# Kernel optimization log

Measured on AMD Instinct MI355X. Metric: run time of the kernel, lower is better.

## Reference

```python
import jax, jax.numpy as jnp
import numpy as np

B, V, S = 16, 100000, 4096
LOSS_WEIGHT = 1.0


def setup_inputs() -> dict:
    key = jax.random.key(0)
    k1, k2, k3, k4 = jax.random.split(key, 4)
    return {
        "src_verts": jax.random.normal(k1, (B, V, 3), dtype=jnp.float32),
        "dst_verts": jax.random.normal(k2, (B, V, 3), dtype=jnp.float32),
        "src_idx": jax.random.randint(k3, (B, S), 0, V, dtype=jnp.int64),
        "dst_idx": jax.random.randint(k4, (B, S), 0, V, dtype=jnp.int64),
    }


def _gather(verts, idx):
    # verts: (B, V, 3), idx: (B, S) -> (B, S, 3)
    return jnp.take_along_axis(verts, idx[:, :, None], axis=1)


def reference(src_verts, dst_verts, src_idx, dst_idx):
    src = _gather(src_verts, src_idx)  # (B, S, 3)
    dst = _gather(dst_verts, dst_idx)  # (B, S, 3)
    # squared euclidean distance matrix, matching torch.cdist(p=2)**2
    s2 = jnp.sum(src * src, axis=-1)  # (B, S)
    d2 = jnp.sum(dst * dst, axis=-1)  # (B, S)
    gram = jnp.einsum("bsc,btc->bst", src, dst)  # (B, S, S)
    dist_mat = jnp.maximum(s2[:, :, None] + d2[:, None, :] - 2.0 * gram, 0.0)
    # min over src points (dim=1) + min over dst points (dim=2)
    chamfer_distance = jnp.min(dist_mat, axis=1) + jnp.min(dist_mat, axis=2)  # (B, S)
    chamfer_loss = jnp.mean(chamfer_distance, axis=-1)  # (B,)
    chamfer_loss = jnp.mean(chamfer_loss, axis=0)  # scalar ('mean' reduction)
    return chamfer_loss * LOSS_WEIGHT
```

## Files before the change

### kernel.cpp

```cpp
#include <hip/hip_runtime.h>
#include <hip/hip_bf16.h>
#include <math.h>

#define B 16
#define V 100000
#define S 4096
#define BS (B * S)
#define NT 512
#define JP 16
#define ONE_BF 0x3F80u

typedef __attribute__((ext_vector_type(8))) short bf16x8;
typedef __attribute__((ext_vector_type(16))) float f32x16;

static __device__ __forceinline__ unsigned bft(float x) {
  return __float_as_uint(x) >> 16;
}
static __device__ __forceinline__ float bff(unsigned hbits) {
  return __uint_as_float(hbits << 16);
}
static __device__ __forceinline__ unsigned pk(unsigned lo, unsigned hi) {
  return (lo & 0xFFFFu) | (hi << 16);
}


__global__ __launch_bounds__(NT) void chamfer_prep_kernel(
    const float* __restrict__ src_verts, const float* __restrict__ dst_verts,
    const int* __restrict__ src_idx, const int* __restrict__ dst_idx,
    uint2* __restrict__ srcfrag, uint4* __restrict__ dstfrag,
    float* __restrict__ out) {
  int t = blockIdx.x * NT + threadIdx.x;
  if (t == 0) *out = 0.f;
  int set = t >> 16;
  int i = t & (BS - 1);
  int b = i >> 12;

  const int* idx = set ? dst_idx : src_idx;
  const float* verts = set ? dst_verts : src_verts;
  int v = idx[i];
  v = v < 0 ? 0 : (v >= V ? V - 1 : v);
  const float* pv = verts + ((size_t)b * V + v) * 3;
  float x = pv[0], y = pv[1], z = pv[2];
  unsigned hx = bft(x), hy = bft(y), hz = bft(z);
  float n2 = x * x + y * y + z * z;
  unsigned n2h = bft(n2);
  unsigned n2l = bft(n2 - bff(n2h));

  if (set == 0) {
    unsigned lx = bft(x - bff(hx)), ly = bft(y - bff(hy)), lz = bft(z - bff(hz));
    int tile = i >> 5, c = i & 31;
    uint2* base = srcfrag + (size_t)tile * 128;
    base[c]      = make_uint2(pk(hx, hy), pk(hz, lx));
    base[64 + c] = make_uint2(pk(ly, lz), pk(hx, hy));
    base[32 + c] = make_uint2(pk(hz, n2h), pk(n2l, ONE_BF));
    base[96 + c] = make_uint2(pk(ONE_BF, 0u), 0u);
  } else {
    unsigned mx = bft(-2.f * bff(hx)), my = bft(-2.f * bff(hy)), mz = bft(-2.f * bff(hz));
    unsigned nx = bft(-2.f * (x - bff(hx)));
    unsigned ny = bft(-2.f * (y - bff(hy)));
    unsigned nz = bft(-2.f * (z - bff(hz)));
    dstfrag[(size_t)i * 2]     = make_uint4(pk(mx, my), pk(mz, mx), pk(my, mz), pk(nx, ny));
    dstfrag[(size_t)i * 2 + 1] = make_uint4(pk(nz, ONE_BF), pk(ONE_BF, n2h), pk(n2l, 0u), 0u);
  }
}

__global__ __launch_bounds__(NT, 4) void chamfer_mfma_kernel(
    const uint4* __restrict__ srcfrag4, const uint4* __restrict__ dstfrag,
    float* __restrict__ part_src, float* __restrict__ part_dst) {
  __shared__ struct {
    uint4 sfrag[2048];
    unsigned smin[1024];
  } sh;
  float* red = (float*)sh.sfrag;

  int bid = blockIdx.x;
  int b = bid >> 6;
  int jp = (bid >> 2) & 15;
  int iq = bid & 3;
  int tid = threadIdx.x;

  const uint4* chunk = srcfrag4 + (size_t)(b * S + iq * 1024) * 2;
  #pragma unroll
  for (int k = 0; k < 4; ++k) {
    sh.sfrag[tid + k * NT] = chunk[tid + k * NT];
  }
  for (int p = tid; p < 1024; p += NT) sh.smin[p] = 0x7F800000u;

  int w = tid >> 6;
  int lane = tid & 63;
  int c = lane & 31, h = lane >> 5;
  int gj = b * S + jp * 256 + w * 32 + c;
  bf16x8 A = __builtin_bit_cast(bf16x8, dstfrag[(size_t)gj * 2 + h]);

  __syncthreads();

  const uint2* sf2 = (const uint2*)sh.sfrag;
  f32x16 zero = {};
  f32x16 mn;
  #pragma unroll
  for (int r = 0; r < 16; ++r) mn[r] = INFINITY;

  int t0r = 4 * w;
  #pragma unroll 4
  for (int it = 0; it < 32; ++it) {
    int t = (it + t0r) & 31;
    uint2 u0 = sf2[t * 128 + lane];
    uint2 u1 = sf2[t * 128 + 64 + lane];
    bf16x8 Bf = __builtin_bit_cast(bf16x8, make_uint4(u0.x, u0.y, u1.x, u1.y));
    f32x16 d = __builtin_amdgcn_mfma_f32_32x32x16_bf16(A, Bf, zero, 0, 0, 0);
    #pragma unroll
    for (int r = 0; r < 16; ++r) mn[r] = fminf(mn[r], d[r]);
    float t0 = fminf(fminf(d[0], d[1]), d[2]);
    float t1 = fminf(fminf(d[3], d[4]), d[5]);
    float t2 = fminf(fminf(d[6], d[7]), d[8]);
    float t3 = fminf(fminf(d[9], d[10]), d[11]);
    float t4 = fminf(fminf(d[12], d[13]), d[14]);
    float m = fminf(fminf(fminf(t0, t1), fminf(t2, t3)), fminf(t4, d[15]));
    atomicMin(&sh.smin[t * 32 + c], __float_as_uint(fmaxf(m, 0.f)));
  }

  __syncthreads();
  for (int p = tid; p < 1024; p += NT) {
    part_src[jp * BS + b * S + iq * 1024 + p] = __uint_as_float(sh.smin[p]);
  }
  __syncthreads();

  #pragma unroll
  for (int r = 0; r < 16; ++r) {
    int row = w * 32 + (r & 3) + 8 * (r >> 2) + 4 * h;
    red[row * 33 + c] = mn[r];
  }
  __syncthreads();
  {
    int row = tid >> 1, half = tid & 1;
    const float* rp = red + row * 33 + half * 16;
    float a0 = fminf(fminf(rp[0], rp[1]), rp[2]);
    float a1 = fminf(fminf(rp[3], rp[4]), rp[5]);
    float a2 = fminf(fminf(rp[6], rp[7]), rp[8]);
    float a3 = fminf(fminf(rp[9], rp[10]), rp[11]);
    float a4 = fminf(fminf(rp[12], rp[13]), rp[14]);
    float m = fminf(fminf(fminf(a0, a1), fminf(a2, a3)), fminf(a4, rp[15]));
    m = fminf(m, __shfl_xor(m, 1, 64));
    if (half == 0) {
      part_dst[iq * BS + b * S + jp * 256 + row] = fmaxf(m, 0.f);
    }
  }
}

__global__ __launch_bounds__(256) void chamfer_reduce_kernel(
    const float* __restrict__ parts, float* __restrict__ out) {
  __shared__ float red[4];
  int tid = threadIdx.x;
  int i4 = blockIdx.x * 256 + tid;

  const float4* ps = (const float4*)parts;
  const float4* pd = (const float4*)(parts + 16 * BS);

  float4 ms = ps[i4];
  #pragma unroll
  for (int j = 1; j < 16; ++j) {
    float4 t = ps[j * (BS / 4) + i4];
    ms.x = fminf(ms.x, t.x); ms.y = fminf(ms.y, t.y);
    ms.z = fminf(ms.z, t.z); ms.w = fminf(ms.w, t.w);
  }
  float4 md = pd[i4];
  #pragma unroll
  for (int j = 1; j < 4; ++j) {
    float4 t = pd[j * (BS / 4) + i4];
    md.x = fminf(md.x, t.x); md.y = fminf(md.y, t.y);
    md.z = fminf(md.z, t.z); md.w = fminf(md.w, t.w);
  }
  float v = (ms.x + ms.y + ms.z + ms.w) + (md.x + md.y + md.z + md.w);
  v *= (1.0f / (float)BS);

  #pragma unroll
  for (int off = 32; off > 0; off >>= 1) v += __shfl_down(v, off, 64);
  if ((tid & 63) == 0) red[tid >> 6] = v;
  __syncthreads();
  if (tid == 0) atomicAdd(out, (red[0] + red[1]) + (red[2] + red[3]));
}

extern "C" void kernel_launch(void* const* d_in, const int* in_sizes, int n_in,
                              void* d_out, int out_size, void* d_ws, size_t ws_size,
                              hipStream_t stream) {
  const float* src_verts = (const float*)d_in[0];
  const float* dst_verts = (const float*)d_in[1];
  const int* src_idx = (const int*)d_in[2];
  const int* dst_idx = (const int*)d_in[3];
  float* out = (float*)d_out;

  float* parts = (float*)d_ws;
  float* part_src = parts;
  float* part_dst = parts + 16 * BS;
  uint2* srcfrag = (uint2*)(parts + 21 * BS);
  uint4* dstfrag = (uint4*)(parts + 29 * BS);

  chamfer_prep_kernel<<<2 * BS / NT, NT, 0, stream>>>(
      src_verts, dst_verts, src_idx, dst_idx, srcfrag, dstfrag, out);

  chamfer_mfma_kernel<<<B * JP * 4, NT, 0, stream>>>(
      (const uint4*)srcfrag, dstfrag, part_src, part_dst);

  chamfer_reduce_kernel<<<64, 256, 0, stream>>>(parts, out);
}
```

Baseline: 33.19 us.

## Compute two MFMA row tiles per wave with 256 threads and one 16-byte B fragment read

The MFMA kernel now runs 256 threads per block. Each wave holds two A fragments covering 64 dst rows, so every B fragment read from LDS feeds two MFMAs. The src fragment layout is repacked so each lane loads a single uint4 instead of two uint2 values, and one atomicMin per tile now covers both MFMAs. The aim is to cut LDS traffic and LDS atomics per unit of MFMA work, at the cost of more accumulator registers and fewer waves per block.

```diff
diff --git a/kernel.cpp b/kernel.cpp
--- a/kernel.cpp
+++ b/kernel.cpp
@@ -6,8 +6,7 @@
 #define V 100000
 #define S 4096
 #define BS (B * S)
-#define NT 512
-#define JP 16
+#define NT 256
 #define ONE_BF 0x3F80u
 
 typedef __attribute__((ext_vector_type(8))) short bf16x8;
@@ -24,12 +23,12 @@
 }
 
 
-__global__ __launch_bounds__(NT) void chamfer_prep_kernel(
+__global__ __launch_bounds__(512) void chamfer_prep_kernel(
     const float* __restrict__ src_verts, const float* __restrict__ dst_verts,
     const int* __restrict__ src_idx, const int* __restrict__ dst_idx,
-    uint2* __restrict__ srcfrag, uint4* __restrict__ dstfrag,
+    uint4* __restrict__ srcfrag, uint4* __restrict__ dstfrag,
     float* __restrict__ out) {
-  int t = blockIdx.x * NT + threadIdx.x;
+  int t = blockIdx.x * 512 + threadIdx.x;
   if (t == 0) *out = 0.f;
   int set = t >> 16;
   int i = t & (BS - 1);
@@ -49,11 +48,9 @@
   if (set == 0) {
     unsigned lx = bft(x - bff(hx)), ly = bft(y - bff(hy)), lz = bft(z - bff(hz));
     int tile = i >> 5, c = i & 31;
-    uint2* base = srcfrag + (size_t)tile * 128;
-    base[c]      = make_uint2(pk(hx, hy), pk(hz, lx));
-    base[64 + c] = make_uint2(pk(ly, lz), pk(hx, hy));
-    base[32 + c] = make_uint2(pk(hz, n2h), pk(n2l, ONE_BF));
-    base[96 + c] = make_uint2(pk(ONE_BF, 0u), 0u);
+    uint4* base = srcfrag + (size_t)tile * 64;
+    base[c]      = make_uint4(pk(hx, hy), pk(hz, lx), pk(ly, lz), pk(hx, hy));
+    base[32 + c] = make_uint4(pk(hz, n2h), pk(n2l, ONE_BF), pk(ONE_BF, 0u), 0u);
   } else {
     unsigned mx = bft(-2.f * bff(hx)), my = bft(-2.f * bff(hy)), mz = bft(-2.f * bff(hz));
     unsigned nx = bft(-2.f * (x - bff(hx)));
@@ -65,7 +62,7 @@
 }
 
 __global__ __launch_bounds__(NT, 4) void chamfer_mfma_kernel(
-    const uint4* __restrict__ srcfrag4, const uint4* __restrict__ dstfrag,
+    const uint4* __restrict__ srcfrag, const uint4* __restrict__ dstfrag,
     float* __restrict__ part_src, float* __restrict__ part_dst) {
   __shared__ struct {
     uint4 sfrag[2048];
@@ -79,71 +76,88 @@
   int iq = bid & 3;
   int tid = threadIdx.x;
 
-  const uint4* chunk = srcfrag4 + (size_t)(b * S + iq * 1024) * 2;
-  #pragma unroll
-  for (int k = 0; k < 4; ++k) {
+  const uint4* chunk = srcfrag + (size_t)(b * 128 + iq * 32) * 64;
+  #pragma unroll
+  for (int k = 0; k < 8; ++k) {
     sh.sfrag[tid + k * NT] = chunk[tid + k * NT];
   }
-  for (int p = tid; p < 1024; p += NT) sh.smin[p] = 0x7F800000u;
+  #pragma unroll
+  for (int k = 0; k < 4; ++k) sh.smin[tid + k * NT] = 0x7F800000u;
 
   int w = tid >> 6;
   int lane = tid & 63;
   int c = lane & 31, h = lane >> 5;
-  int gj = b * S + jp * 256 + w * 32 + c;
-  bf16x8 A = __builtin_bit_cast(bf16x8, dstfrag[(size_t)gj * 2 + h]);
-
-  __syncthreads();
-
-  const uint2* sf2 = (const uint2*)sh.sfrag;
+  int gj = b * S + jp * 256 + w * 64 + c;
+  bf16x8 A0 = __builtin_bit_cast(bf16x8, dstfrag[(size_t)gj * 2 + h]);
+  bf16x8 A1 = __builtin_bit_cast(bf16x8, dstfrag[(size_t)(gj + 32) * 2 + h]);
+
+  __syncthreads();
+
   f32x16 zero = {};
-  f32x16 mn;
-  #pragma unroll
-  for (int r = 0; r < 16; ++r) mn[r] = INFINITY;
-
-  int t0r = 4 * w;
+  f32x16 mn0, mn1;
+  #pragma unroll
+  for (int r = 0; r < 16; ++r) { mn0[r] = INFINITY; mn1[r] = INFINITY; }
+
+  int t0r = 8 * w;
   #pragma unroll 4
   for (int it = 0; it < 32; ++it) {
     int t = (it + t0r) & 31;
-    uint2 u0 = sf2[t * 128 + lane];
-    uint2 u1 = sf2[t * 128 + 64 + lane];
-    bf16x8 Bf = __builtin_bit_cast(bf16x8, make_uint4(u0.x, u0.y, u1.x, u1.y));
-    f32x16 d = __builtin_amdgcn_mfma_f32_32x32x16_bf16(A, Bf, zero, 0, 0, 0);
+    bf16x8 Bf = __builtin_bit_cast(bf16x8, sh.sfrag[t * 64 + lane]);
+    f32x16 d0 = __builtin_amdgcn_mfma_f32_32x32x16_bf16(A0, Bf, zero, 0, 0, 0);
+    f32x16 d1 = __builtin_amdgcn_mfma_f32_32x32x16_bf16(A1, Bf, zero, 0, 0, 0);
     #pragma unroll
-    for (int r = 0; r < 16; ++r) mn[r] = fminf(mn[r], d[r]);
-    float t0 = fminf(fminf(d[0], d[1]), d[2]);
-    float t1 = fminf(fminf(d[3], d[4]), d[5]);
-    float t2 = fminf(fminf(d[6], d[7]), d[8]);
-    float t3 = fminf(fminf(d[9], d[10]), d[11]);
-    float t4 = fminf(fminf(d[12], d[13]), d[14]);
-    float m = fminf(fminf(fminf(t0, t1), fminf(t2, t3)), fminf(t4, d[15]));
+    for (int r = 0; r < 16; ++r) mn0[r] = fminf(mn0[r], d0[r]);
+    #pragma unroll
+    for (int r = 0; r < 16; ++r) mn1[r] = fminf(mn1[r], d1[r]);
+    float t0 = fminf(fminf(d0[0], d0[1]), d0[2]);
+    float t1 = fminf(fminf(d0[3], d0[4]), d0[5]);
+    float t2 = fminf(fminf(d0[6], d0[7]), d0[8]);
+    float t3 = fminf(fminf(d0[9], d0[10]), d0[11]);
+    float t4 = fminf(fminf(d0[12], d0[13]), d0[14]);
+    float s0 = fminf(fminf(d1[0], d1[1]), d1[2]);
+    float s1 = fminf(fminf(d1[3], d1[4]), d1[5]);
+    float s2 = fminf(fminf(d1[6], d1[7]), d1[8]);
+    float s3 = fminf(fminf(d1[9], d1[10]), d1[11]);
+    float s4 = fminf(fminf(d1[12], d1[13]), d1[14]);
+    float m0 = fminf(fminf(fminf(t0, t1), fminf(t2, t3)), fminf(t4, d0[15]));
+    float m1 = fminf(fminf(fminf(s0, s1), fminf(s2, s3)), fminf(s4, d1[15]));
+    float m = fminf(m0, m1);
     atomicMin(&sh.smin[t * 32 + c], __float_as_uint(fmaxf(m, 0.f)));
   }
 
   __syncthreads();
-  for (int p = tid; p < 1024; p += NT) {
+  #pragma unroll
+  for (int k = 0; k < 4; ++k) {
+    int p = tid + k * NT;
     part_src[jp * BS + b * S + iq * 1024 + p] = __uint_as_float(sh.smin[p]);
   }
   __syncthreads();
 
   #pragma unroll
   for (int r = 0; r < 16; ++r) {
-    int row = w * 32 + (r & 3) + 8 * (r >> 2) + 4 * h;
-    red[row * 33 + c] = mn[r];
+    int row = w * 64 + (r & 3) + 8 * (r >> 2) + 4 * h;
+    red[row * 33 + c] = mn0[r];
+    red[(row + 32) * 33 + c] = mn1[r];
   }
   __syncthreads();
   {
-    int row = tid >> 1, half = tid & 1;
-    const float* rp = red + row * 33 + half * 16;
+    int row = tid;
+    const float* rp = red + row * 33;
     float a0 = fminf(fminf(rp[0], rp[1]), rp[2]);
     float a1 = fminf(fminf(rp[3], rp[4]), rp[5]);
     float a2 = fminf(fminf(rp[6], rp[7]), rp[8]);
     float a3 = fminf(fminf(rp[9], rp[10]), rp[11]);
     float a4 = fminf(fminf(rp[12], rp[13]), rp[14]);
-    float m = fminf(fminf(fminf(a0, a1), fminf(a2, a3)), fminf(a4, rp[15]));
-    m = fminf(m, __shfl_xor(m, 1, 64));
-    if (half == 0) {
-      part_dst[iq * BS + b * S + jp * 256 + row] = fmaxf(m, 0.f);
-    }
+    float a5 = fminf(fminf(rp[15], rp[16]), rp[17]);
+    float a6 = fminf(fminf(rp[18], rp[19]), rp[20]);
+    float a7 = fminf(fminf(rp[21], rp[22]), rp[23]);
+    float a8 = fminf(fminf(rp[24], rp[25]), rp[26]);
+    float a9 = fminf(fminf(rp[27], rp[28]), rp[29]);
+    float aa = fminf(rp[30], rp[31]);
+    float m = fminf(fminf(fminf(fminf(a0, a1), fminf(a2, a3)),
+                          fminf(fminf(a4, a5), fminf(a6, a7))),
+                    fminf(fminf(a8, a9), aa));
+    part_dst[iq * BS + b * S + jp * 256 + row] = fmaxf(m, 0.f);
   }
 }
 
@@ -192,14 +206,14 @@
   float* parts = (float*)d_ws;
   float* part_src = parts;
   float* part_dst = parts + 16 * BS;
-  uint2* srcfrag = (uint2*)(parts + 21 * BS);
+  uint4* srcfrag = (uint4*)(parts + 21 * BS);
   uint4* dstfrag = (uint4*)(parts + 29 * BS);
 
-  chamfer_prep_kernel<<<2 * BS / NT, NT, 0, stream>>>(
+  chamfer_prep_kernel<<<2 * BS / 512, 512, 0, stream>>>(
       src_verts, dst_verts, src_idx, dst_idx, srcfrag, dstfrag, out);
 
-  chamfer_mfma_kernel<<<B * JP * 4, NT, 0, stream>>>(
-      (const uint4*)srcfrag, dstfrag, part_src, part_dst);
+  chamfer_mfma_kernel<<<B * 16 * 4, NT, 0, stream>>>(
+      srcfrag, dstfrag, part_src, part_dst);
 
   chamfer_reduce_kernel<<<64, 256, 0, stream>>>(parts, out);
 }
```

New measurement: 31.46 us. -5.2%, faster.
